# Kernel tuning notes

Measured on AMD Instinct MI355X. Metric: run time of the kernel, lower is better.

## Reference

```python
import jax, jax.numpy as jnp
import numpy as np
import math

HEADS = 4
LN_EPS = 1e-5


def _layer_norm(x, gamma, beta):
    # LayerNorm over last dim (N=4096), matching nn.LayerNorm(4096)
    mu = jnp.mean(x, axis=-1, keepdims=True)
    var = jnp.mean((x - mu) ** 2, axis=-1, keepdims=True)
    return (x - mu) * jax.lax.rsqrt(var + LN_EPS) * gamma + beta


def setup_inputs() -> dict:
    key = jax.random.key(0)
    ks = jax.random.split(key, 10)
    L, IMG, N = 1024, 1024, 4096
    s_img = 1.0 / math.sqrt(IMG)
    s_L = 1.0 / math.sqrt(L)
    return {
        "point_features": jax.random.normal(ks[0], (1, L, N), jnp.float32),
        "img_features": jax.random.normal(ks[1], (1, IMG, N), jnp.float32),
        # 4 per-head 1x1 convs IMG_chl -> L_chl
        "W_img": jax.random.normal(ks[2], (HEADS, L, IMG), jnp.float32) * s_img,
        "b_img": jax.random.normal(ks[3], (HEADS, L), jnp.float32) * s_img,
        # conv_L: L_chl -> L_chl
        "W_L": jax.random.normal(ks[4], (L, L), jnp.float32) * s_L,
        "b_L": jax.random.normal(ks[5], (L,), jnp.float32) * s_L,
        # LayerNorm(4096)
        "ln_g": jnp.ones((N,), jnp.float32),
        "ln_b": jnp.zeros((N,), jnp.float32),
        # conv_fusion: L_chl -> L_chl
        "W_f": jax.random.normal(ks[6], (L, L), jnp.float32) * s_L,
        "b_f": jax.random.normal(ks[7], (L,), jnp.float32) * s_L,
    }


def reference(point_features, img_features, W_img, b_img, W_L, b_L, ln_g, ln_b, W_f, b_f):
    # L_query = conv_L(point_features): [1, L, N]
    L_query = jnp.einsum('oi,bin->bon', W_L, point_features) + b_L[None, :, None]
    dk = L_query.shape[1]
    N = L_query.shape[2]

    # All 4 head keys at once: [H, 1, L, N]
    keys = jnp.einsum('hoi,bin->hbon', W_img, img_features) + b_img[:, None, :, None]

    # score_i = sum_c(key_i * query) / sqrt(dk)  -> cat over heads: [H, N] (B=1)
    score = jnp.sum(keys * L_query[None], axis=2).reshape(HEADS, N) / jnp.sqrt(jnp.float32(dk))

    # softmax across heads (dim=0), weightmap = [1, H, N]
    weight = jax.nn.softmax(score, axis=0)
    weightmap = weight[None]

    # z = sum_h weight[h] * key_h : [1, L, N]
    z = jnp.einsum('hn,hbcn->bcn', weight, keys)

    fused = _layer_norm(z + L_query, ln_g, ln_b)
    fusion_features = jnp.einsum('oi,bin->bon', W_f, fused) + b_f[None, :, None]
    return (fusion_features, weightmap)
```

## Files before the change

### kernel.cpp

```cpp
#include <hip/hip_runtime.h>
#include <hip/hip_bf16.h>
#include <stdint.h>

using u16 = unsigned short;

typedef __attribute__((ext_vector_type(8))) short bf16x8;
typedef __attribute__((ext_vector_type(4))) float f32x4;

typedef const __attribute__((address_space(1))) unsigned int* gas_t;
typedef __attribute__((address_space(3))) unsigned int* las_t;

__device__ inline void g2l16(const u16* g, u16* l) {
  __builtin_amdgcn_global_load_lds((gas_t)g, (las_t)l, 16, 0, 0);
}

__device__ inline u16 f2b(float x) {
  union { float f; uint32_t u; } v; v.f = x;
  uint32_t r = (v.u + 0x7FFFu + ((v.u >> 16) & 1u)) >> 16;
  return (u16)r;
}
__device__ inline float b2f(u16 b) {
  union { uint32_t u; float f; } v; v.u = ((uint32_t)b) << 16;
  return v.f;
}

__device__ inline void store_out(float* p, float v) { *p = v; }
__device__ inline void store_out(u16* p, float v) { *p = f2b(v); }

template<typename OutT>
__global__ __launch_bounds__(256)
void gemm_bt(const u16* __restrict__ A, const u16* __restrict__ Bt,
             const float* __restrict__ bias, OutT* __restrict__ C,
             int M, int N, int K)
{
  __shared__ u16 As[128 * 32];
  __shared__ u16 Bs[128 * 32];

  const int tid  = threadIdx.x;
  const int wave = tid >> 6;
  const int lane = tid & 63;
  const int wm = wave >> 1, wn = wave & 1;
  const int lr = lane & 15;
  const int lq = lane >> 4;

  const int m0 = blockIdx.y * 128;
  const int n0 = blockIdx.x * 128;

  const u16* gA = A  + (size_t)(m0 + (tid >> 2)) * K + ((tid & 3) << 3);
  const u16* gB = Bt + (size_t)(n0 + (tid >> 2)) * K + ((tid & 3) << 3);
  u16* dstA = As + wave * 512;
  u16* dstB = Bs + wave * 512;

  f32x4 acc[4][4];
  #pragma unroll
  for (int i = 0; i < 4; ++i)
    #pragma unroll
    for (int j = 0; j < 4; ++j)
      acc[i][j] = (f32x4){0.f, 0.f, 0.f, 0.f};

  for (int k0 = 0; k0 < K; k0 += 32) {
    g2l16(gA + k0,                dstA);
    g2l16(gA + (size_t)64 * K + k0, dstA + 2048);
    g2l16(gB + k0,                dstB);
    g2l16(gB + (size_t)64 * K + k0, dstB + 2048);
    __syncthreads();

    bf16x8 af[4], bfr[4];
    #pragma unroll
    for (int im = 0; im < 4; ++im)
      af[im] = *(const bf16x8*)&As[(wm * 64 + im * 16 + lr) * 32 + lq * 8];
    #pragma unroll
    for (int in = 0; in < 4; ++in)
      bfr[in] = *(const bf16x8*)&Bs[(wn * 64 + in * 16 + lr) * 32 + lq * 8];

    #pragma unroll
    for (int im = 0; im < 4; ++im)
      #pragma unroll
      for (int in = 0; in < 4; ++in)
        acc[im][in] = __builtin_amdgcn_mfma_f32_16x16x32_bf16(
            af[im], bfr[in], acc[im][in], 0, 0, 0);

    __syncthreads();
  }

  #pragma unroll
  for (int im = 0; im < 4; ++im) {
    const int mbase = m0 + wm * 64 + im * 16 + lq * 4;
    #pragma unroll
    for (int in = 0; in < 4; ++in) {
      const int ncol = n0 + wn * 64 + in * 16 + lr;
      #pragma unroll
      for (int r = 0; r < 4; ++r) {
        const int m = mbase + r;
        store_out(C + (size_t)m * N + ncol, acc[im][in][r] + bias[m]);
      }
    }
  }
}

template<typename OutT>
__global__ __launch_bounds__(256)
void gemm_bt_64(const u16* __restrict__ A, const u16* __restrict__ Bt,
                const float* __restrict__ bias, OutT* __restrict__ C,
                int M, int N, int K)
{
  __shared__ u16 As[64 * 32];
  __shared__ u16 Bs[128 * 32];

  const int tid  = threadIdx.x;
  const int wave = tid >> 6;
  const int lane = tid & 63;
  const int lr = lane & 15;
  const int lq = lane >> 4;

  const int m0 = blockIdx.y * 64;
  const int n0 = blockIdx.x * 128;

  const u16* gA = A  + (size_t)(m0 + (tid >> 2)) * K + ((tid & 3) << 3);
  const u16* gB = Bt + (size_t)(n0 + (tid >> 2)) * K + ((tid & 3) << 3);
  u16* dstA = As + wave * 512;
  u16* dstB = Bs + wave * 512;

  f32x4 acc[4][2];
  #pragma unroll
  for (int i = 0; i < 4; ++i)
    #pragma unroll
    for (int j = 0; j < 2; ++j)
      acc[i][j] = (f32x4){0.f, 0.f, 0.f, 0.f};

  for (int k0 = 0; k0 < K; k0 += 32) {
    g2l16(gA + k0,                  dstA);
    g2l16(gB + k0,                  dstB);
    g2l16(gB + (size_t)64 * K + k0, dstB + 2048);
    __syncthreads();

    bf16x8 af[4], bfr[2];
    #pragma unroll
    for (int im = 0; im < 4; ++im)
      af[im] = *(const bf16x8*)&As[(im * 16 + lr) * 32 + lq * 8];
    #pragma unroll
    for (int in = 0; in < 2; ++in)
      bfr[in] = *(const bf16x8*)&Bs[(wave * 32 + in * 16 + lr) * 32 + lq * 8];

    #pragma unroll
    for (int im = 0; im < 4; ++im)
      #pragma unroll
      for (int in = 0; in < 2; ++in)
        acc[im][in] = __builtin_amdgcn_mfma_f32_16x16x32_bf16(
            af[im], bfr[in], acc[im][in], 0, 0, 0);

    __syncthreads();
  }

  #pragma unroll
  for (int im = 0; im < 4; ++im) {
    const int mbase = m0 + im * 16 + lq * 4;
    #pragma unroll
    for (int in = 0; in < 2; ++in) {
      const int ncol = n0 + wave * 32 + in * 16 + lr;
      #pragma unroll
      for (int r = 0; r < 4; ++r) {
        const int m = mbase + r;
        store_out(C + (size_t)m * N + ncol, acc[im][in][r] + bias[m]);
      }
    }
  }
}

__global__ __launch_bounds__(256)
void cast_transpose(const float* __restrict__ in, u16* __restrict__ out,
                    int R, int C)
{
  __shared__ u16 tile[32][33];
  const int c0 = blockIdx.x * 32, r0 = blockIdx.y * 32;
  const int tx = threadIdx.x & 31, ty = threadIdx.x >> 5;
  #pragma unroll
  for (int k = 0; k < 4; ++k)
    tile[ty + 8 * k][tx] = f2b(in[(size_t)(r0 + ty + 8 * k) * C + c0 + tx]);
  __syncthreads();
  #pragma unroll
  for (int k = 0; k < 4; ++k)
    out[(size_t)(c0 + ty + 8 * k) * R + r0 + tx] = tile[tx][ty + 8 * k];
}

__global__ __launch_bounds__(256)
void transpose_u16(const u16* __restrict__ in, u16* __restrict__ out,
                   int R, int C)
{
  __shared__ u16 tile[32][33];
  const int c0 = blockIdx.x * 32, r0 = blockIdx.y * 32;
  const int tx = threadIdx.x & 31, ty = threadIdx.x >> 5;
  #pragma unroll
  for (int k = 0; k < 4; ++k)
    tile[ty + 8 * k][tx] = in[(size_t)(r0 + ty + 8 * k) * C + c0 + tx];
  __syncthreads();
  #pragma unroll
  for (int k = 0; k < 4; ++k)
    out[(size_t)(c0 + ty + 8 * k) * R + r0 + tx] = tile[tx][ty + 8 * k];
}

__global__ __launch_bounds__(256)
void cast_f32_bf16(const float4* __restrict__ in, ushort4* __restrict__ out,
                   int n4)
{
  const int i = blockIdx.x * 256 + threadIdx.x;
  if (i >= n4) return;
  const float4 v = in[i];
  ushort4 o;
  o.x = f2b(v.x); o.y = f2b(v.y); o.z = f2b(v.z); o.w = f2b(v.w);
  out[i] = o;
}

__global__ __launch_bounds__(256)
void score_partial(const u16* __restrict__ keys, const float* __restrict__ Q,
                   float* __restrict__ score)
{
  const int n  = blockIdx.x * 256 + threadIdx.x;
  const int c0 = blockIdx.y * 128;
  float s[4] = {0.f, 0.f, 0.f, 0.f};
  for (int c = c0; c < c0 + 128; ++c) {
    const float q = Q[(size_t)c * 4096 + n];
    #pragma unroll
    for (int h = 0; h < 4; ++h)
      s[h] = fmaf(q, b2f(keys[((size_t)((h << 10) + c)) * 4096 + n]), s[h]);
  }
  #pragma unroll
  for (int h = 0; h < 4; ++h)
    atomicAdd(&score[h * 4096 + n], s[h] * 0.03125f);
}

__global__ __launch_bounds__(256)
void softmax_h(const float* __restrict__ score, float* __restrict__ wmap)
{
  const int n = blockIdx.x * 256 + threadIdx.x;
  const float s0 = score[n], s1 = score[4096 + n];
  const float s2 = score[8192 + n], s3 = score[12288 + n];
  const float m = fmaxf(fmaxf(s0, s1), fmaxf(s2, s3));
  const float e0 = expf(s0 - m), e1 = expf(s1 - m);
  const float e2 = expf(s2 - m), e3 = expf(s3 - m);
  const float inv = 1.f / (e0 + e1 + e2 + e3);
  wmap[n] = e0 * inv; wmap[4096 + n] = e1 * inv;
  wmap[8192 + n] = e2 * inv; wmap[12288 + n] = e3 * inv;
}

__global__ __launch_bounds__(256)
void z_ln(const u16* __restrict__ keys, const float* __restrict__ Q,
          const float* __restrict__ w, const float* __restrict__ g,
          const float* __restrict__ bb, u16* __restrict__ fused)
{
  const int c  = blockIdx.x;
  const int tx = threadIdx.x;
  float t[16];
  float s = 0.f, s2 = 0.f;
  #pragma unroll
  for (int j = 0; j < 16; ++j) {
    const int n = tx + j * 256;
    const float q = Q[(size_t)c * 4096 + n];
    float z = 0.f;
    #pragma unroll
    for (int h = 0; h < 4; ++h)
      z = fmaf(w[h * 4096 + n], b2f(keys[((size_t)((h << 10) + c)) * 4096 + n]), z);
    const float v = z + q;
    t[j] = v; s += v; s2 = fmaf(v, v, s2);
  }
  #pragma unroll
  for (int o = 32; o > 0; o >>= 1) {
    s  += __shfl_down(s, o);
    s2 += __shfl_down(s2, o);
  }
  __shared__ float rbuf[8];
  const int wave = tx >> 6, lane = tx & 63;
  if (lane == 0) { rbuf[wave] = s; rbuf[4 + wave] = s2; }
  __syncthreads();
  s  = rbuf[0] + rbuf[1] + rbuf[2] + rbuf[3];
  s2 = rbuf[4] + rbuf[5] + rbuf[6] + rbuf[7];
  const float mu  = s * (1.f / 4096.f);
  const float var = s2 * (1.f / 4096.f) - mu * mu;
  const float rs  = rsqrtf(var + 1e-5f);
  #pragma unroll
  for (int j = 0; j < 16; ++j) {
    const int n = tx + j * 256;
    fused[(size_t)c * 4096 + n] = f2b((t[j] - mu) * rs * g[n] + bb[n]);
  }
}

extern "C" void kernel_launch(void* const* d_in, const int* in_sizes, int n_in,
                              void* d_out, int out_size, void* d_ws, size_t ws_size,
                              hipStream_t stream)
{
  const float* P   = (const float*)d_in[0];
  const float* I   = (const float*)d_in[1];
  const float* Wim = (const float*)d_in[2];
  const float* bim = (const float*)d_in[3];
  const float* WL  = (const float*)d_in[4];
  const float* bL  = (const float*)d_in[5];
  const float* lng = (const float*)d_in[6];
  const float* lnb = (const float*)d_in[7];
  const float* Wf  = (const float*)d_in[8];
  const float* bf_ = (const float*)d_in[9];
  float* out = (float*)d_out;

  char* ws = (char*)d_ws;
  u16*   PT     = (u16*)(ws + 0);
  u16*   IT     = (u16*)(ws + (size_t)8  * 1048576);
  u16*   WLb    = (u16*)(ws + (size_t)16 * 1048576);
  u16*   WIb    = (u16*)(ws + (size_t)18 * 1048576);
  u16*   WFb    = (u16*)(ws + (size_t)26 * 1048576);
  float* Q      = (float*)(ws + (size_t)28 * 1048576);
  u16*   KEYS   = (u16*)(ws + (size_t)44 * 1048576);
  float* SCORE  = (float*)(ws + (size_t)76 * 1048576);
  u16*   FUSED  = (u16*)(ws + (size_t)77 * 1048576);
  u16*   FUSEDT = (u16*)(ws + (size_t)85 * 1048576);

  const dim3 b256(256);

  cast_transpose<<<dim3(128, 32), b256, 0, stream>>>(P, PT, 1024, 4096);
  cast_transpose<<<dim3(128, 32), b256, 0, stream>>>(I, IT, 1024, 4096);
  cast_f32_bf16<<<1024, b256, 0, stream>>>((const float4*)WL,  (ushort4*)WLb, 262144);
  cast_f32_bf16<<<4096, b256, 0, stream>>>((const float4*)Wim, (ushort4*)WIb, 1048576);
  cast_f32_bf16<<<1024, b256, 0, stream>>>((const float4*)Wf,  (ushort4*)WFb, 262144);

  gemm_bt_64<float><<<dim3(32, 16), b256, 0, stream>>>(WLb, PT, bL, Q, 1024, 4096, 1024);
  gemm_bt<u16><<<dim3(32, 32), b256, 0, stream>>>(WIb, IT, bim, KEYS, 4096, 4096, 1024);

  hipMemsetAsync(SCORE, 0, 4 * 4096 * sizeof(float), stream);
  score_partial<<<dim3(16, 8), b256, 0, stream>>>(KEYS, Q, SCORE);
  float* wmap = out + (size_t)1024 * 4096;
  softmax_h<<<16, b256, 0, stream>>>(SCORE, wmap);

  z_ln<<<1024, b256, 0, stream>>>(KEYS, Q, wmap, lng, lnb, FUSED);
  transpose_u16<<<dim3(128, 32), b256, 0, stream>>>(FUSED, FUSEDT, 1024, 4096);

  gemm_bt_64<float><<<dim3(32, 16), b256, 0, stream>>>(WFb, FUSEDT, bf_, out, 1024, 4096, 1024);
}
```

Before: 254.9 us.

## Deepen GEMM K-tile with XOR-swizzled LDS, merge cast kernels, drop score atomics

Result: faster. 232.0 us (-9.0%).

```diff
diff --git a/kernel.cpp b/kernel.cpp
--- a/kernel.cpp
+++ b/kernel.cpp
@@ -33,8 +33,8 @@
              const float* __restrict__ bias, OutT* __restrict__ C,
              int M, int N, int K)
 {
-  __shared__ u16 As[128 * 32];
-  __shared__ u16 Bs[128 * 32];
+  __shared__ u16 As[128 * 64];
+  __shared__ u16 Bs[128 * 64];
 
   const int tid  = threadIdx.x;
   const int wave = tid >> 6;
@@ -42,12 +42,15 @@
   const int wm = wave >> 1, wn = wave & 1;
   const int lr = lane & 15;
   const int lq = lane >> 4;
+  const int x7 = lr & 7;
 
   const int m0 = blockIdx.y * 128;
   const int n0 = blockIdx.x * 128;
 
-  const u16* gA = A  + (size_t)(m0 + (tid >> 2)) * K + ((tid & 3) << 3);
-  const u16* gB = Bt + (size_t)(n0 + (tid >> 2)) * K + ((tid & 3) << 3);
+  const int srow = tid >> 3;
+  const int sgc  = (tid & 7) ^ (srow & 7);
+  const u16* gA = A  + (size_t)(m0 + srow) * K + sgc * 8;
+  const u16* gB = Bt + (size_t)(n0 + srow) * K + sgc * 8;
   u16* dstA = As + wave * 512;
   u16* dstB = Bs + wave * 512;
 
@@ -58,28 +61,32 @@
     for (int j = 0; j < 4; ++j)
       acc[i][j] = (f32x4){0.f, 0.f, 0.f, 0.f};
 
-  for (int k0 = 0; k0 < K; k0 += 32) {
-    g2l16(gA + k0,                dstA);
-    g2l16(gA + (size_t)64 * K + k0, dstA + 2048);
-    g2l16(gB + k0,                dstB);
-    g2l16(gB + (size_t)64 * K + k0, dstB + 2048);
+  for (int k0 = 0; k0 < K; k0 += 64) {
+    #pragma unroll
+    for (int s = 0; s < 4; ++s) {
+      g2l16(gA + (size_t)(s * 32) * K + k0, dstA + s * 2048);
+      g2l16(gB + (size_t)(s * 32) * K + k0, dstB + s * 2048);
+    }
     __syncthreads();
 
-    bf16x8 af[4], bfr[4];
-    #pragma unroll
-    for (int im = 0; im < 4; ++im)
-      af[im] = *(const bf16x8*)&As[(wm * 64 + im * 16 + lr) * 32 + lq * 8];
-    #pragma unroll
-    for (int in = 0; in < 4; ++in)
-      bfr[in] = *(const bf16x8*)&Bs[(wn * 64 + in * 16 + lr) * 32 + lq * 8];
-
-    #pragma unroll
-    for (int im = 0; im < 4; ++im)
+    #pragma unroll
+    for (int ks = 0; ks < 2; ++ks) {
+      const int pa = (ks * 4 + lq) ^ x7;
+      bf16x8 af[4], bfr[4];
+      #pragma unroll
+      for (int im = 0; im < 4; ++im)
+        af[im] = *(const bf16x8*)&As[(wm * 64 + im * 16 + lr) * 64 + pa * 8];
       #pragma unroll
       for (int in = 0; in < 4; ++in)
-        acc[im][in] = __builtin_amdgcn_mfma_f32_16x16x32_bf16(
-            af[im], bfr[in], acc[im][in], 0, 0, 0);
-
+        bfr[in] = *(const bf16x8*)&Bs[(wn * 64 + in * 16 + lr) * 64 + pa * 8];
+
+      #pragma unroll
+      for (int im = 0; im < 4; ++im)
+        #pragma unroll
+        for (int in = 0; in < 4; ++in)
+          acc[im][in] = __builtin_amdgcn_mfma_f32_16x16x32_bf16(
+              af[im], bfr[in], acc[im][in], 0, 0, 0);
+    }
     __syncthreads();
   }
 
@@ -104,20 +111,23 @@
                 const float* __restrict__ bias, OutT* __restrict__ C,
                 int M, int N, int K)
 {
-  __shared__ u16 As[64 * 32];
-  __shared__ u16 Bs[128 * 32];
+  __shared__ u16 As[64 * 64];
+  __shared__ u16 Bs[128 * 64];
 
   const int tid  = threadIdx.x;
   const int wave = tid >> 6;
   const int lane = tid & 63;
   const int lr = lane & 15;
   const int lq = lane >> 4;
+  const int x7 = lr & 7;
 
   const int m0 = blockIdx.y * 64;
   const int n0 = blockIdx.x * 128;
 
-  const u16* gA = A  + (size_t)(m0 + (tid >> 2)) * K + ((tid & 3) << 3);
-  const u16* gB = Bt + (size_t)(n0 + (tid >> 2)) * K + ((tid & 3) << 3);
+  const int srow = tid >> 3;
+  const int sgc  = (tid & 7) ^ (srow & 7);
+  const u16* gA = A  + (size_t)(m0 + srow) * K + sgc * 8;
+  const u16* gB = Bt + (size_t)(n0 + srow) * K + sgc * 8;
   u16* dstA = As + wave * 512;
   u16* dstB = Bs + wave * 512;
 
@@ -128,27 +138,33 @@
     for (int j = 0; j < 2; ++j)
       acc[i][j] = (f32x4){0.f, 0.f, 0.f, 0.f};
 
-  for (int k0 = 0; k0 < K; k0 += 32) {
-    g2l16(gA + k0,                  dstA);
-    g2l16(gB + k0,                  dstB);
-    g2l16(gB + (size_t)64 * K + k0, dstB + 2048);
+  for (int k0 = 0; k0 < K; k0 += 64) {
+    #pragma unroll
+    for (int s = 0; s < 2; ++s)
+      g2l16(gA + (size_t)(s * 32) * K + k0, dstA + s * 2048);
+    #pragma unroll
+    for (int s = 0; s < 4; ++s)
+      g2l16(gB + (size_t)(s * 32) * K + k0, dstB + s * 2048);
     __syncthreads();
 
-    bf16x8 af[4], bfr[2];
-    #pragma unroll
-    for (int im = 0; im < 4; ++im)
-      af[im] = *(const bf16x8*)&As[(im * 16 + lr) * 32 + lq * 8];
-    #pragma unroll
-    for (int in = 0; in < 2; ++in)
-      bfr[in] = *(const bf16x8*)&Bs[(wave * 32 + in * 16 + lr) * 32 + lq * 8];
-
-    #pragma unroll
-    for (int im = 0; im < 4; ++im)
+    #pragma unroll
+    for (int ks = 0; ks < 2; ++ks) {
+      const int pa = (ks * 4 + lq) ^ x7;
+      bf16x8 af[4], bfr[2];
+      #pragma unroll
+      for (int im = 0; im < 4; ++im)
+        af[im] = *(const bf16x8*)&As[(im * 16 + lr) * 64 + pa * 8];
       #pragma unroll
       for (int in = 0; in < 2; ++in)
-        acc[im][in] = __builtin_amdgcn_mfma_f32_16x16x32_bf16(
-            af[im], bfr[in], acc[im][in], 0, 0, 0);
-
+        bfr[in] = *(const bf16x8*)&Bs[(wave * 32 + in * 16 + lr) * 64 + pa * 8];
+
+      #pragma unroll
+      for (int im = 0; im < 4; ++im)
+        #pragma unroll
+        for (int in = 0; in < 2; ++in)
+          acc[im][in] = __builtin_amdgcn_mfma_f32_16x16x32_bf16(
+              af[im], bfr[in], acc[im][in], 0, 0, 0);
+    }
     __syncthreads();
   }
 
@@ -168,9 +184,12 @@
 }
 
 __global__ __launch_bounds__(256)
-void cast_transpose(const float* __restrict__ in, u16* __restrict__ out,
-                    int R, int C)
-{
+void cast_transpose2(const float* __restrict__ in0, u16* __restrict__ out0,
+                     const float* __restrict__ in1, u16* __restrict__ out1,
+                     int R, int C)
+{
+  const float* in = blockIdx.z ? in1 : in0;
+  u16* out = blockIdx.z ? out1 : out0;
   __shared__ u16 tile[32][33];
   const int c0 = blockIdx.x * 32, r0 = blockIdx.y * 32;
   const int tx = threadIdx.x & 31, ty = threadIdx.x >> 5;
@@ -200,23 +219,28 @@
 }
 
 __global__ __launch_bounds__(256)
-void cast_f32_bf16(const float4* __restrict__ in, ushort4* __restrict__ out,
-                   int n4)
-{
-  const int i = blockIdx.x * 256 + threadIdx.x;
-  if (i >= n4) return;
-  const float4 v = in[i];
+void cast_weights(const float4* __restrict__ wim, const float4* __restrict__ wl,
+                  const float4* __restrict__ wf, ushort4* __restrict__ wimb,
+                  ushort4* __restrict__ wlb, ushort4* __restrict__ wfb)
+{
+  int i = blockIdx.x * 256 + threadIdx.x;
+  const float4* src; ushort4* dst;
+  if (i < 1048576)      { src = wim; dst = wimb; }
+  else if (i < 1310720) { src = wl;  dst = wlb;  i -= 1048576; }
+  else                  { src = wf;  dst = wfb;  i -= 1310720; }
+  const float4 v = src[i];
   ushort4 o;
   o.x = f2b(v.x); o.y = f2b(v.y); o.z = f2b(v.z); o.w = f2b(v.w);
-  out[i] = o;
+  dst[i] = o;
 }
 
 __global__ __launch_bounds__(256)
 void score_partial(const u16* __restrict__ keys, const float* __restrict__ Q,
-                   float* __restrict__ score)
+                   float* __restrict__ spart)
 {
   const int n  = blockIdx.x * 256 + threadIdx.x;
-  const int c0 = blockIdx.y * 128;
+  const int cb = blockIdx.y;
+  const int c0 = cb * 128;
   float s[4] = {0.f, 0.f, 0.f, 0.f};
   for (int c = c0; c < c0 + 128; ++c) {
     const float q = Q[(size_t)c * 4096 + n];
@@ -226,18 +250,24 @@
   }
   #pragma unroll
   for (int h = 0; h < 4; ++h)
-    atomicAdd(&score[h * 4096 + n], s[h] * 0.03125f);
-}
-
-__global__ __launch_bounds__(256)
-void softmax_h(const float* __restrict__ score, float* __restrict__ wmap)
+    spart[((size_t)cb * 4 + h) * 4096 + n] = s[h];
+}
+
+__global__ __launch_bounds__(256)
+void softmax_h(const float* __restrict__ spart, float* __restrict__ wmap)
 {
   const int n = blockIdx.x * 256 + threadIdx.x;
-  const float s0 = score[n], s1 = score[4096 + n];
-  const float s2 = score[8192 + n], s3 = score[12288 + n];
-  const float m = fmaxf(fmaxf(s0, s1), fmaxf(s2, s3));
-  const float e0 = expf(s0 - m), e1 = expf(s1 - m);
-  const float e2 = expf(s2 - m), e3 = expf(s3 - m);
+  float s[4] = {0.f, 0.f, 0.f, 0.f};
+  #pragma unroll
+  for (int cb = 0; cb < 8; ++cb)
+    #pragma unroll
+    for (int h = 0; h < 4; ++h)
+      s[h] += spart[((size_t)cb * 4 + h) * 4096 + n];
+  #pragma unroll
+  for (int h = 0; h < 4; ++h) s[h] *= 0.03125f;
+  const float m = fmaxf(fmaxf(s[0], s[1]), fmaxf(s[2], s[3]));
+  const float e0 = expf(s[0] - m), e1 = expf(s[1] - m);
+  const float e2 = expf(s[2] - m), e3 = expf(s[3] - m);
   const float inv = 1.f / (e0 + e1 + e2 + e3);
   wmap[n] = e0 * inv; wmap[4096 + n] = e1 * inv;
   wmap[8192 + n] = e2 * inv; wmap[12288 + n] = e3 * inv;
@@ -308,25 +338,23 @@
   u16*   WFb    = (u16*)(ws + (size_t)26 * 1048576);
   float* Q      = (float*)(ws + (size_t)28 * 1048576);
   u16*   KEYS   = (u16*)(ws + (size_t)44 * 1048576);
-  float* SCORE  = (float*)(ws + (size_t)76 * 1048576);
+  float* SPART  = (float*)(ws + (size_t)76 * 1048576);
   u16*   FUSED  = (u16*)(ws + (size_t)77 * 1048576);
   u16*   FUSEDT = (u16*)(ws + (size_t)85 * 1048576);
 
   const dim3 b256(256);
 
-  cast_transpose<<<dim3(128, 32), b256, 0, stream>>>(P, PT, 1024, 4096);
-  cast_transpose<<<dim3(128, 32), b256, 0, stream>>>(I, IT, 1024, 4096);
-  cast_f32_bf16<<<1024, b256, 0, stream>>>((const float4*)WL,  (ushort4*)WLb, 262144);
-  cast_f32_bf16<<<4096, b256, 0, stream>>>((const float4*)Wim, (ushort4*)WIb, 1048576);
-  cast_f32_bf16<<<1024, b256, 0, stream>>>((const float4*)Wf,  (ushort4*)WFb, 262144);
+  cast_transpose2<<<dim3(128, 32, 2), b256, 0, stream>>>(P, PT, I, IT, 1024, 4096);
+  cast_weights<<<6144, b256, 0, stream>>>((const float4*)Wim, (const float4*)WL,
+                                          (const float4*)Wf, (ushort4*)WIb,
+                                          (ushort4*)WLb, (ushort4*)WFb);
 
   gemm_bt_64<float><<<dim3(32, 16), b256, 0, stream>>>(WLb, PT, bL, Q, 1024, 4096, 1024);
   gemm_bt<u16><<<dim3(32, 32), b256, 0, stream>>>(WIb, IT, bim, KEYS, 4096, 4096, 1024);
 
-  hipMemsetAsync(SCORE, 0, 4 * 4096 * sizeof(float), stream);
-  score_partial<<<dim3(16, 8), b256, 0, stream>>>(KEYS, Q, SCORE);
+  score_partial<<<dim3(16, 8), b256, 0, stream>>>(KEYS, Q, SPART);
   float* wmap = out + (size_t)1024 * 4096;
-  softmax_h<<<16, b256, 0, stream>>>(SCORE, wmap);
+  softmax_h<<<16, b256, 0, stream>>>(SPART, wmap);
 
   z_ln<<<1024, b256, 0, stream>>>(KEYS, Q, wmap, lng, lnb, FUSED);
   transpose_u16<<<dim3(128, 32), b256, 0, stream>>>(FUSED, FUSEDT, 1024, 4096);
```
